# Kernel tuning notes

Measured on AMD Instinct MI355X. Metric: run time of the kernel, lower is better.

## Reference

```python
import jax, jax.numpy as jnp
import numpy as np

C = 1.0      # base manifold curvature (Lorentz c)
C_E = 1.0    # expert manifold curvature (all experts init to c=1.0)
K = 1        # n_activated_experts (top-k)
SCALE = 2.0  # LResNet scale for shared-expert combine
EPS = 1e-8


def _lorentz_swiglu(x, W1, W3, W2, c_mid, c_out, prescale):
    """LorentzExpert / LorentzFeedForward: SwiGLU on space coords with Lorentz time lift.
    x: [T, D] (full Lorentz vector). W1,W3: [I-1, D]; W2: [D-1, I]. Returns [T, D]."""
    if prescale:
        x = x * np.float32(np.sqrt(C_E / C))  # x * sqrt(c_expert / c)
    s1 = jax.nn.silu(x @ W1.T)                 # [T, I-1] w1(x, return_space=True)
    s3 = x @ W3.T                              # [T, I-1] w3(x, return_space=True)
    sp = s1 * s3                               # gated space part
    t = jnp.sqrt(jnp.clip((sp * sp).sum(-1, keepdims=True) + c_mid, EPS))
    h = jnp.concatenate([t, sp], axis=-1)      # [T, I] point on expert manifold
    o = h @ W2.T                               # [T, D-1] w2 space output
    ot = jnp.sqrt(jnp.clip((o * o).sum(-1, keepdims=True) + c_out, EPS))
    return jnp.concatenate([ot, o], axis=-1)   # [T, D] on base manifold


def setup_inputs() -> dict:
    key = jax.random.key(0)
    ks = jax.random.split(key, 9)
    T, D, E, I = 2048, 1024, 8, 1024
    x = jax.random.normal(ks[0], (T, D), jnp.float32)
    gate_w = jax.random.normal(ks[1], (E, D - 1), jnp.float32) / np.sqrt(D - 1)
    gate_b = jax.random.normal(ks[2], (E,), jnp.float32) * 0.01
    W1 = jax.random.normal(ks[3], (E, I - 1, D), jnp.float32) / np.sqrt(D)
    W3 = jax.random.normal(ks[4], (E, I - 1, D), jnp.float32) / np.sqrt(D)
    W2 = jax.random.normal(ks[5], (E, D - 1, I), jnp.float32) / np.sqrt(I)
    Ws1 = jax.random.normal(ks[6], (I - 1, D), jnp.float32) / np.sqrt(D)
    Ws3 = jax.random.normal(ks[7], (I - 1, D), jnp.float32) / np.sqrt(D)
    Ws2 = jax.random.normal(ks[8], (D - 1, I), jnp.float32) / np.sqrt(I)
    return {"x": x, "gate_w": gate_w, "gate_b": gate_b, "W1": W1, "W3": W3,
            "W2": W2, "Ws1": Ws1, "Ws3": Ws3, "Ws2": Ws2}


def reference(x, gate_w, gate_b, W1, W3, W2, Ws1, Ws3, Ws2):
    T, D = x.shape
    E = gate_w.shape[0]
    # ---- Gate (softmax scoring, n_groups == 1, route_scale == 1.0) ----
    logits = x[:, 1:] @ gate_w.T                                    # [T, E]
    scores = jax.nn.softmax(logits.astype(jnp.float32), axis=-1)
    biased = scores + gate_b                                        # bias only affects routing
    _, idx = jax.lax.top_k(biased, K)                               # [T, K]
    weights = jnp.take_along_axis(scores, idx, axis=-1).astype(x.dtype)  # [T, K]
    # dense per-token expert gate weights [T, E]
    oh = jax.nn.one_hot(idx, E, dtype=x.dtype)                      # [T, K, E]
    gw = (oh * weights[..., None]).sum(axis=1)                      # [T, E]
    # ---- y init: project(zeros) -> [sqrt(c), 0, ..., 0] ----
    y0 = jnp.concatenate([jnp.full((T, 1), np.sqrt(C), x.dtype),
                          jnp.zeros((T, D - 1), x.dtype)], axis=-1)
    # ---- routed experts (dense reference: every expert on every token, masked combine) ----
    e_out = jax.vmap(lambda w1, w3, w2: _lorentz_swiglu(x, w1, w3, w2, C_E, C, True))(W1, W3, W2)  # [E, T, D]
    y = y0 + jnp.einsum('te,etd->td', gw, e_out)
    # ---- shared expert (LorentzFeedForward, stays on base manifold) ----
    z = _lorentz_swiglu(x, Ws1, Ws3, Ws2, C, C, False)
    # ---- LResNet weighted sum: normalize (z + scale*y) back to manifold ----
    comb = z + SCALE * y
    li = (comb[:, 1:] ** 2).sum(-1, keepdims=True) - comb[:, :1] ** 2  # Lorentz inner <comb,comb>
    out = np.float32(np.sqrt(C)) * comb / jnp.sqrt(jnp.clip(jnp.abs(li), EPS))
    return out
```

## Files before the change

### kernel.cpp

```cpp
#include <hip/hip_runtime.h>

typedef __bf16 bf16;
typedef __attribute__((ext_vector_type(8))) __bf16 bf16x8;
typedef __attribute__((ext_vector_type(4))) float floatx4;

#define TOK 2048
#define DD  1024
#define NE  8
#define SMAX 24

#define MFMA16(A,B,C) __builtin_amdgcn_mfma_f32_16x16x32_bf16(A,B,C,0,0,0)

__device__ __forceinline__ void load_lds16(const bf16* g, bf16* l) {
  __builtin_amdgcn_global_load_lds(
      (const __attribute__((address_space(1))) void*)g,
      (__attribute__((address_space(3))) void*)l, 16, 0, 0);
}

#define WBAR(N) asm volatile("s_waitcnt vmcnt(" #N ")\n\ts_barrier" ::: "memory")
#define BARO    asm volatile("s_barrier" ::: "memory")

__device__ __forceinline__ uint4 pack_bf8(float4 a, float4 b) {
  union { bf16 h[8]; uint4 u; } p;
  p.h[0] = (bf16)a.x; p.h[1] = (bf16)a.y; p.h[2] = (bf16)a.z; p.h[3] = (bf16)a.w;
  p.h[4] = (bf16)b.x; p.h[5] = (bf16)b.y; p.h[6] = (bf16)b.z; p.h[7] = (bf16)b.w;
  return p.u;
}

#define NCVT (8*2046 + 2046 + 8*1023 + 1023)
__global__ __launch_bounds__(128) void convert_kernel(
    const float* __restrict__ W1, const float* __restrict__ W3,
    const float* __restrict__ W2, const float* __restrict__ Ws1,
    const float* __restrict__ Ws3, const float* __restrict__ Ws2,
    bf16* __restrict__ w13, bf16* __restrict__ ws13,
    bf16* __restrict__ w2b, bf16* __restrict__ ws2b)
{
  const int r = blockIdx.x, tid = threadIdx.x;
  const float* src; bf16* dst;
  if (r < 8 * 2046) {
    const int e = r / 2046, q = r % 2046;
    src = ((q & 1) ? W3 : W1) + ((size_t)e * 1023 + (q >> 1)) * 1024;
    dst = w13 + (size_t)r * 1024;
  } else if (r < 8 * 2046 + 2046) {
    const int q = r - 8 * 2046;
    src = ((q & 1) ? Ws3 : Ws1) + (size_t)(q >> 1) * 1024;
    dst = ws13 + (size_t)q * 1024;
  } else if (r < 8 * 2046 + 2046 + 8 * 1023) {
    const int q = r - (8 * 2046 + 2046);
    src = W2 + (size_t)q * 1024;
    dst = w2b + (size_t)q * 1024;
  } else {
    const int q = r - (8 * 2046 + 2046 + 8 * 1023);
    src = Ws2 + (size_t)q * 1024;
    dst = ws2b + (size_t)q * 1024;
  }
  const float4 f0 = ((const float4*)src)[tid * 2];
  const float4 f1 = ((const float4*)src)[tid * 2 + 1];
  ((uint4*)dst)[tid] = pack_bf8(f0, f1);
}

__global__ __launch_bounds__(256) void gate_cvt_kernel(
    const float* __restrict__ x, const float* __restrict__ gate_w,
    const float* __restrict__ gate_b, bf16* __restrict__ x_bf,
    int* __restrict__ eidx, float* __restrict__ ewgt, float* __restrict__ ss)
{
  const int t = blockIdx.x, tid = threadIdx.x;
  if (tid < 4) ss[tid * TOK + t] = 0.f;
  const float4 v = ((const float4*)(x + (size_t)t * DD))[tid];
  union { bf16 h[4]; uint2 u; } pk;
  pk.h[0] = (bf16)v.x; pk.h[1] = (bf16)v.y; pk.h[2] = (bf16)v.z; pk.h[3] = (bf16)v.w;
  ((uint2*)(x_bf + (size_t)t * DD))[tid] = pk.u;

  float acc[NE];
#pragma unroll
  for (int e = 0; e < NE; ++e) acc[e] = 0.f;
  const float vv[4] = {v.x, v.y, v.z, v.w};
#pragma unroll
  for (int i = 0; i < 4; ++i) {
    const int d = tid * 4 + i;
    if (d >= 1) {
#pragma unroll
      for (int e = 0; e < NE; ++e) acc[e] += vv[i] * gate_w[e * (DD - 1) + d - 1];
    }
  }
#pragma unroll
  for (int off = 32; off > 0; off >>= 1) {
#pragma unroll
    for (int e = 0; e < NE; ++e) acc[e] += __shfl_down(acc[e], off);
  }
  __shared__ float red[4][NE];
  const int wid = tid >> 6, lane = tid & 63;
  if (lane == 0) {
#pragma unroll
    for (int e = 0; e < NE; ++e) red[wid][e] = acc[e];
  }
  __syncthreads();
  if (tid == 0) {
    float lg[NE];
#pragma unroll
    for (int e = 0; e < NE; ++e) lg[e] = red[0][e] + red[1][e] + red[2][e] + red[3][e];
    float m = lg[0];
    for (int e = 1; e < NE; ++e) m = fmaxf(m, lg[e]);
    float ex[NE], s = 0.f;
    for (int e = 0; e < NE; ++e) { ex[e] = expf(lg[e] - m); s += ex[e]; }
    const float inv = 1.f / s;
    int best = 0; float bb = ex[0] * inv + gate_b[0];
    for (int e = 1; e < NE; ++e) {
      const float b = ex[e] * inv + gate_b[e];
      if (b > bb) { bb = b; best = e; }
    }
    eidx[t] = best;
    ewgt[t] = ex[best] * inv;
  }
}

__global__ __launch_bounds__(256) void route_kernel(
    const int* __restrict__ eidx, int* __restrict__ perm,
    int* __restrict__ pos_of, int4* __restrict__ wl, int* __restrict__ n1)
{
  __shared__ int cnt[NE], off[NE], bas[NE + 1];
  const int tid = threadIdx.x;
  if (tid < NE) cnt[tid] = 0;
  __syncthreads();
  for (int t = tid; t < TOK; t += 256) atomicAdd(&cnt[eidx[t]], 1);
  __syncthreads();
  if (tid == 0) {
    int run = 0;
    for (int e = 0; e < NE; ++e) { bas[e] = run; off[e] = run; run += cnt[e]; }
    bas[NE] = run;
    int n = 0;
    for (int e = 0; e < NE; ++e)
      for (int r0 = 0; r0 < cnt[e]; r0 += 256) {
        int rows = cnt[e] - r0; if (rows > 256) rows = 256;
        wl[n++] = make_int4(bas[e] + r0, rows, e, 0);
      }
    for (int r0 = 0; r0 < TOK; r0 += 256) wl[n++] = make_int4(r0, 256, NE, 0);
    *n1 = n;
  }
  __syncthreads();
  for (int t = tid; t < TOK; t += 256) {
    const int e = eidx[t];
    const int p = atomicAdd(&off[e], 1);
    perm[p] = t;
    pos_of[t] = p;
  }
}

__global__ __launch_bounds__(1024) void mlp1_kernel(
    const bf16* __restrict__ x_bf, const bf16* __restrict__ w13,
    const bf16* __restrict__ ws13,
    const int* __restrict__ perm, const int4* __restrict__ wl,
    const int* __restrict__ wl_n,
    bf16* __restrict__ h_r, bf16* __restrict__ h_s,
    float* __restrict__ ss_r, float* __restrict__ ss_z)
{
  const int bid = blockIdx.x;
  const int slot = bid % SMAX, nt = bid / SMAX;
  if (slot >= *wl_n) return;
  const int4 wle = wl[slot];
  const int mbase = wle.x, rows = wle.y, eid = wle.z;
  const int tid = threadIdx.x;
  const bool routed = (eid < NE);
  const bf16* bmat = routed ? w13 + (size_t)eid * 2046 * 1024 : ws13;
  bf16* hbuf  = routed ? h_r : h_s;
  float* ssbuf = routed ? ss_r : ss_z;

  extern __shared__ __align__(16) bf16 smem[];
  bf16* const Asb[2] = {smem, smem + 16384};
  bf16* const Bsb[2] = {smem + 32768, smem + 49152};
  __shared__ int toks[256];
  if (tid < 256) {
    int r = tid < rows ? tid : rows - 1;
    toks[tid] = routed ? perm[mbase + r] : (mbase + r);
  }
  __syncthreads();

  const int wid = tid >> 6, lane = tid & 63;
  const int srow = lane >> 3;
  const int kbg  = (lane & 7) ^ (srow & 7);
  const bf16 *aG0, *aG1, *bG0, *bG1;
  int aL0o, aL1o, bL0o, bL1o;
  {
    const int r0 = wid * 16;
    aG0 = x_bf + (size_t)toks[r0 + 0 + srow] * 1024 + kbg * 8;
    aG1 = x_bf + (size_t)toks[r0 + 8 + srow] * 1024 + kbg * 8;
    aL0o = (r0 + 0) * 64; aL1o = (r0 + 8) * 64;
    int b0 = nt * 256 + r0 + 0 + srow; if (b0 > 2045) b0 = 2045;
    int b1 = nt * 256 + r0 + 8 + srow; if (b1 > 2045) b1 = 2045;
    bG0 = bmat + (size_t)b0 * 1024 + kbg * 8;
    bG1 = bmat + (size_t)b1 * 1024 + kbg * 8;
    bL0o = (r0 + 0) * 64; bL1o = (r0 + 8) * 64;
  }

  const int lrow = lane & 15, quad = lane >> 4, sw = lane & 7;
  const int wrow = (wid >> 2) * 64, wcol = (wid & 3) * 64;
  int aoff[4], boff[4], koff[2];
#pragma unroll
  for (int mi = 0; mi < 4; ++mi) aoff[mi] = (wrow + mi * 16 + lrow) * 64;
#pragma unroll
  for (int ni = 0; ni < 4; ++ni) boff[ni] = (wcol + ni * 16 + lrow) * 64;
#pragma unroll
  for (int kk = 0; kk < 2; ++kk) koff[kk] = ((kk * 4 + quad) ^ sw) * 8;

  const floatx4 fz = {0.f, 0.f, 0.f, 0.f};
  floatx4 acc[4][4];
#pragma unroll
  for (int mi = 0; mi < 4; ++mi)
#pragma unroll
    for (int ni = 0; ni < 4; ++ni) acc[mi][ni] = fz;

#define STAGE1(KE, BUF) { \
    load_lds16(aG0 + (KE), Asb[BUF] + aL0o); load_lds16(aG1 + (KE), Asb[BUF] + aL1o); \
    load_lds16(bG0 + (KE), Bsb[BUF] + bL0o); load_lds16(bG1 + (KE), Bsb[BUF] + bL1o); }

#define COMP1(BUF) { \
_Pragma("unroll") \
    for (int kk = 0; kk < 2; ++kk) { \
      bf16x8 av[4], bv[4]; \
_Pragma("unroll") \
      for (int mi = 0; mi < 4; ++mi) av[mi] = *(const bf16x8*)(Asb[BUF] + aoff[mi] + koff[kk]); \
_Pragma("unroll") \
      for (int ni = 0; ni < 4; ++ni) bv[ni] = *(const bf16x8*)(Bsb[BUF] + boff[ni] + koff[kk]); \
_Pragma("unroll") \
      for (int mi = 0; mi < 4; ++mi) \
_Pragma("unroll") \
        for (int ni = 0; ni < 4; ++ni) \
          acc[mi][ni] = MFMA16(av[mi], bv[ni], acc[mi][ni]); \
    } }

  STAGE1(0, 0)
  STAGE1(64, 1)
#pragma unroll 1
  for (int t = 0; t < 7; ++t) {
    const int ke = t * 128;
    WBAR(4); COMP1(0) BARO; STAGE1(ke + 128, 0)
    WBAR(4); COMP1(1) BARO; STAGE1(ke + 192, 1)
  }
  WBAR(4); COMP1(0)
  WBAR(0); COMP1(1)
#undef STAGE1
#undef COMP1

#pragma unroll
  for (int mi = 0; mi < 4; ++mi) {
#pragma unroll
    for (int r = 0; r < 4; ++r) {
      const int row = wrow + mi * 16 + quad * 4 + r;
      const bool rowok = row < rows;
      float ssum = 0.f;
#pragma unroll
      for (int ni = 0; ni < 4; ++ni) {
        const float c = acc[mi][ni][r];
        const float partner = __shfl_xor(c, 1);
        const float s1 = (lane & 1) ? partner : c;
        const float s3 = (lane & 1) ? c : partner;
        const float sp = (s1 / (1.f + __expf(-s1))) * s3;
        const int P = (nt * 256 + wcol + ni * 16 + lrow) >> 1;
        const bool ok = rowok && ((lane & 1) == 0) && (P < 1023);
        if (ok) hbuf[(size_t)(mbase + row) * 1024 + 1 + P] = (bf16)sp;
        ssum += ok ? sp * sp : 0.f;
      }
      ssum += __shfl_xor(ssum, 1);
      ssum += __shfl_xor(ssum, 2);
      ssum += __shfl_xor(ssum, 4);
      ssum += __shfl_xor(ssum, 8);
      if (lrow == 0 && rowok) atomicAdd(ssbuf + mbase + row, ssum);
    }
  }
}

__global__ __launch_bounds__(256) void finalize_t_kernel(
    const float* __restrict__ ss_r, const float* __restrict__ ss_z,
    bf16* __restrict__ h_r, bf16* __restrict__ h_s)
{
  const int i = blockIdx.x * 256 + threadIdx.x;
  if (i < TOK) {
    h_r[(size_t)i * 1024] = (bf16)sqrtf(ss_r[i] + 1.0f);
    h_s[(size_t)i * 1024] = (bf16)sqrtf(ss_z[i] + 1.0f);
  }
}

__global__ __launch_bounds__(1024) void mlp2_kernel(
    const bf16* __restrict__ h_r, const bf16* __restrict__ h_s,
    const bf16* __restrict__ w2b, const bf16* __restrict__ ws2b,
    const int4* __restrict__ wl, const int* __restrict__ wl_n,
    float* __restrict__ o_r, float* __restrict__ o_s,
    float* __restrict__ ss_or, float* __restrict__ ss_oz)
{
  const int bid = blockIdx.x;
  const int slot = bid % SMAX, nt = bid / SMAX;
  if (slot >= *wl_n) return;
  const int4 wle = wl[slot];
  const int mbase = wle.x, rows = wle.y, eid = wle.z;
  const int tid = threadIdx.x;
  const bool routed = (eid < NE);
  const bf16* abuf = routed ? h_r : h_s;
  const bf16* bmat = routed ? w2b + (size_t)eid * 1023 * 1024 : ws2b;
  float* obuf  = routed ? o_r : o_s;
  float* ssbuf = routed ? ss_or : ss_oz;
  const int n0 = nt * 256;

  extern __shared__ __align__(16) bf16 smem[];
  bf16* const Asb[2] = {smem, smem + 16384};
  bf16* const Bsb[2] = {smem + 32768, smem + 49152};

  const int wid = tid >> 6, lane = tid & 63;
  const int srow = lane >> 3;
  const int kbg  = (lane & 7) ^ (srow & 7);
  const bf16 *aG0, *aG1, *bG0, *bG1;
  int aL0o, aL1o, bL0o, bL1o;
  {
    const int r0 = wid * 16;
    int ra0 = r0 + 0 + srow; if (ra0 >= rows) ra0 = rows - 1;
    int ra1 = r0 + 8 + srow; if (ra1 >= rows) ra1 = rows - 1;
    aG0 = abuf + (size_t)(mbase + ra0) * 1024 + kbg * 8;
    aG1 = abuf + (size_t)(mbase + ra1) * 1024 + kbg * 8;
    aL0o = (r0 + 0) * 64; aL1o = (r0 + 8) * 64;
    int b0 = n0 + r0 + 0 + srow; if (b0 > 1022) b0 = 1022;
    int b1 = n0 + r0 + 8 + srow; if (b1 > 1022) b1 = 1022;
    bG0 = bmat + (size_t)b0 * 1024 + kbg * 8;
    bG1 = bmat + (size_t)b1 * 1024 + kbg * 8;
    bL0o = (r0 + 0) * 64; bL1o = (r0 + 8) * 64;
  }

  const int lrow = lane & 15, quad = lane >> 4, sw = lane & 7;
  const int wrow = (wid >> 2) * 64, wcol = (wid & 3) * 64;
  int aoff[4], boff[4], koff[2];
#pragma unroll
  for (int mi = 0; mi < 4; ++mi) aoff[mi] = (wrow + mi * 16 + lrow) * 64;
#pragma unroll
  for (int ni = 0; ni < 4; ++ni) boff[ni] = (wcol + ni * 16 + lrow) * 64;
#pragma unroll
  for (int kk = 0; kk < 2; ++kk) koff[kk] = ((kk * 4 + quad) ^ sw) * 8;

  const floatx4 fz = {0.f, 0.f, 0.f, 0.f};
  floatx4 acc[4][4];
#pragma unroll
  for (int mi = 0; mi < 4; ++mi)
#pragma unroll
    for (int ni = 0; ni < 4; ++ni) acc[mi][ni] = fz;

#define STAGE2(KE, BUF) { \
    load_lds16(aG0 + (KE), Asb[BUF] + aL0o); load_lds16(aG1 + (KE), Asb[BUF] + aL1o); \
    load_lds16(bG0 + (KE), Bsb[BUF] + bL0o); load_lds16(bG1 + (KE), Bsb[BUF] + bL1o); }

#define COMP2(BUF) { \
_Pragma("unroll") \
    for (int kk = 0; kk < 2; ++kk) { \
      bf16x8 av[4], bv[4]; \
_Pragma("unroll") \
      for (int mi = 0; mi < 4; ++mi) av[mi] = *(const bf16x8*)(Asb[BUF] + aoff[mi] + koff[kk]); \
_Pragma("unroll") \
      for (int ni = 0; ni < 4; ++ni) bv[ni] = *(const bf16x8*)(Bsb[BUF] + boff[ni] + koff[kk]); \
_Pragma("unroll") \
      for (int mi = 0; mi < 4; ++mi) \
_Pragma("unroll") \
        for (int ni = 0; ni < 4; ++ni) \
          acc[mi][ni] = MFMA16(av[mi], bv[ni], acc[mi][ni]); \
    } }

  STAGE2(0, 0)
  STAGE2(64, 1)
#pragma unroll 1
  for (int t = 0; t < 7; ++t) {
    const int ke = t * 128;
    WBAR(4); COMP2(0) BARO; STAGE2(ke + 128, 0)
    WBAR(4); COMP2(1) BARO; STAGE2(ke + 192, 1)
  }
  WBAR(4); COMP2(0)
  WBAR(0); COMP2(1)
#undef STAGE2
#undef COMP2

#pragma unroll
  for (int mi = 0; mi < 4; ++mi) {
#pragma unroll
    for (int r = 0; r < 4; ++r) {
      const int row = wrow + mi * 16 + quad * 4 + r;
      const bool rowok = row < rows;
      float ssum = 0.f;
#pragma unroll
      for (int ni = 0; ni < 4; ++ni) {
        const float v = acc[mi][ni][r];
        const int n = n0 + wcol + ni * 16 + lrow;
        const bool ok = rowok && (n < 1023);
        if (ok) obuf[(size_t)(mbase + row) * 1024 + n] = v;
        ssum += ok ? v * v : 0.f;
      }
      ssum += __shfl_xor(ssum, 1);
      ssum += __shfl_xor(ssum, 2);
      ssum += __shfl_xor(ssum, 4);
      ssum += __shfl_xor(ssum, 8);
      if (lrow == 0 && rowok) atomicAdd(ssbuf + mbase + row, ssum);
    }
  }
}

__global__ __launch_bounds__(256) void combine_kernel(
    const float* __restrict__ o_r, const float* __restrict__ o_s,
    const float* __restrict__ ss_or, const float* __restrict__ ss_oz,
    const int* __restrict__ pos_of, const float* __restrict__ wgt,
    float* __restrict__ out)
{
  const int t = blockIdx.x, tid = threadIdx.x;
  const int p = pos_of[t];
  const float w = wgt[t];
  const float4 oz = ((const float4*)(o_s + (size_t)t * 1024))[tid];
  const float4 oe = ((const float4*)(o_r + (size_t)p * 1024))[tid];
  const float tw = 2.f * w;
  float c0 = oz.x + tw * oe.x;
  float c1 = oz.y + tw * oe.y;
  float c2 = oz.z + tw * oe.z;
  float c3 = (tid == 255) ? 0.f : (oz.w + tw * oe.w);
  float ssum = c0 * c0 + c1 * c1 + c2 * c2 + c3 * c3;
#pragma unroll
  for (int off = 32; off > 0; off >>= 1) ssum += __shfl_down(ssum, off);
  __shared__ float rs[4];
  if ((tid & 63) == 0) rs[tid >> 6] = ssum;
  __syncthreads();
  const float space2 = rs[0] + rs[1] + rs[2] + rs[3];
  const float comb0 = sqrtf(ss_oz[t] + 1.f) + 2.f + 2.f * w * sqrtf(ss_or[p] + 1.f);
  const float li = space2 - comb0 * comb0;
  const float inv = 1.f / sqrtf(fmaxf(fabsf(li), 1e-8f));
  float* orow = out + (size_t)t * 1024;
  const int j = 1 + tid * 4;
  orow[j]     = c0 * inv;
  orow[j + 1] = c1 * inv;
  orow[j + 2] = c2 * inv;
  if (tid != 255) orow[j + 3] = c3 * inv;
  if (tid == 0) orow[0] = comb0 * inv;
}

extern "C" void kernel_launch(void* const* d_in, const int* in_sizes, int n_in,
                              void* d_out, int out_size, void* d_ws, size_t ws_size,
                              hipStream_t stream) {
  const float* x      = (const float*)d_in[0];
  const float* gate_w = (const float*)d_in[1];
  const float* gate_b = (const float*)d_in[2];
  const float* W1     = (const float*)d_in[3];
  const float* W3     = (const float*)d_in[4];
  const float* W2     = (const float*)d_in[5];
  const float* Ws1    = (const float*)d_in[6];
  const float* Ws3    = (const float*)d_in[7];
  const float* Ws2    = (const float*)d_in[8];
  float* out = (float*)d_out;

  char* ws = (char*)d_ws;
  size_t off = 0;
  auto alloc = [&](size_t bytes) {
    void* p = ws + off;
    off += (bytes + 255) & ~(size_t)255;
    return p;
  };
  bf16*  x_bf = (bf16*) alloc((size_t)TOK * 1024 * 2);
  bf16*  h_r  = (bf16*) alloc((size_t)TOK * 1024 * 2);
  bf16*  h_s  = (bf16*) alloc((size_t)TOK * 1024 * 2);
  float* o_r  = (float*)alloc((size_t)TOK * 1024 * 4);
  float* o_s  = (float*)alloc((size_t)TOK * 1024 * 4);
  float* ss   = (float*)alloc((size_t)4 * TOK * 4);
  int*   eidx = (int*)  alloc((size_t)TOK * 4);
  float* ewgt = (float*)alloc((size_t)TOK * 4);
  int*   perm = (int*)  alloc((size_t)TOK * 4);
  int*   posf = (int*)  alloc((size_t)TOK * 4);
  int4*  wl1  = (int4*) alloc((size_t)SMAX * 16);
  int*   wn   = (int*)  alloc(32);
  bf16*  w13  = (bf16*) alloc((size_t)8 * 2046 * 1024 * 2);
  bf16*  ws13 = (bf16*) alloc((size_t)2046 * 1024 * 2);
  bf16*  w2b  = (bf16*) alloc((size_t)8 * 1023 * 1024 * 2);
  bf16*  ws2b = (bf16*) alloc((size_t)1023 * 1024 * 2);

  float* ss_r  = ss;
  float* ss_z  = ss + TOK;
  float* ss_or = ss + 2 * TOK;
  float* ss_oz = ss + 3 * TOK;

  const int MLP_LDS = 2 * (256 * 64 + 256 * 64) * 2;
  (void)hipFuncSetAttribute((const void*)mlp1_kernel,
                            hipFuncAttributeMaxDynamicSharedMemorySize, MLP_LDS);
  (void)hipFuncSetAttribute((const void*)mlp2_kernel,
                            hipFuncAttributeMaxDynamicSharedMemorySize, MLP_LDS);

  convert_kernel<<<NCVT, 128, 0, stream>>>(W1, W3, W2, Ws1, Ws3, Ws2,
                                           w13, ws13, w2b, ws2b);
  gate_cvt_kernel<<<TOK, 256, 0, stream>>>(x, gate_w, gate_b, x_bf, eidx, ewgt, ss);
  route_kernel<<<1, 256, 0, stream>>>(eidx, perm, posf, wl1, wn);
  mlp1_kernel<<<8 * SMAX, 1024, MLP_LDS, stream>>>(x_bf, w13, ws13, perm, wl1, wn,
                                                   h_r, h_s, ss_r, ss_z);
  finalize_t_kernel<<<8, 256, 0, stream>>>(ss_r, ss_z, h_r, h_s);
  mlp2_kernel<<<4 * SMAX, 1024, MLP_LDS, stream>>>(h_r, h_s, w2b, ws2b, wl1, wn,
                                                   o_r, o_s, ss_or, ss_oz);
  combine_kernel<<<TOK, 256, 0, stream>>>(o_r, o_s, ss_or, ss_oz, posf, ewgt, out);
}
```

Baseline: 246.1 us.

## Split-K the second MLP GEMM with atomic accumulation and merge prep kernels

The second MLP GEMM is split into two K halves, which doubles the grid and accumulates partial results into zeroed output buffers with float atomics. Because those outputs are now partial, the output squared-norm reduction moves into the combine kernel. The weight conversion, gate and zeroing work are merged into one prep kernel with 256-thread blocks that each convert one row of 1024 floats. The aim is better CU occupancy for the small mlp2 grid and fewer launches, at the cost of extra zeroing traffic and contended atomic writes.

```diff
diff --git a/kernel.cpp b/kernel.cpp
--- a/kernel.cpp
+++ b/kernel.cpp
@@ -20,52 +20,59 @@
 #define WBAR(N) asm volatile("s_waitcnt vmcnt(" #N ")\n\ts_barrier" ::: "memory")
 #define BARO    asm volatile("s_barrier" ::: "memory")
 
-__device__ __forceinline__ uint4 pack_bf8(float4 a, float4 b) {
-  union { bf16 h[8]; uint4 u; } p;
-  p.h[0] = (bf16)a.x; p.h[1] = (bf16)a.y; p.h[2] = (bf16)a.z; p.h[3] = (bf16)a.w;
-  p.h[4] = (bf16)b.x; p.h[5] = (bf16)b.y; p.h[6] = (bf16)b.z; p.h[7] = (bf16)b.w;
-  return p.u;
-}
-
 #define NCVT (8*2046 + 2046 + 8*1023 + 1023)
-__global__ __launch_bounds__(128) void convert_kernel(
+#define GATEB TOK
+#define ZEROB TOK
+__global__ __launch_bounds__(256) void prep_kernel(
+    const float* __restrict__ x, const float* __restrict__ gate_w,
+    const float* __restrict__ gate_b,
     const float* __restrict__ W1, const float* __restrict__ W3,
     const float* __restrict__ W2, const float* __restrict__ Ws1,
     const float* __restrict__ Ws3, const float* __restrict__ Ws2,
+    bf16* __restrict__ x_bf, int* __restrict__ eidx, float* __restrict__ ewgt,
+    float* __restrict__ ss,
     bf16* __restrict__ w13, bf16* __restrict__ ws13,
-    bf16* __restrict__ w2b, bf16* __restrict__ ws2b)
+    bf16* __restrict__ w2b, bf16* __restrict__ ws2b,
+    float* __restrict__ o_r, float* __restrict__ o_s)
 {
-  const int r = blockIdx.x, tid = threadIdx.x;
-  const float* src; bf16* dst;
-  if (r < 8 * 2046) {
-    const int e = r / 2046, q = r % 2046;
-    src = ((q & 1) ? W3 : W1) + ((size_t)e * 1023 + (q >> 1)) * 1024;
-    dst = w13 + (size_t)r * 1024;
-  } else if (r < 8 * 2046 + 2046) {
-    const int q = r - 8 * 2046;
-    src = ((q & 1) ? Ws3 : Ws1) + (size_t)(q >> 1) * 1024;
-    dst = ws13 + (size_t)q * 1024;
-  } else if (r < 8 * 2046 + 2046 + 8 * 1023) {
-    const int q = r - (8 * 2046 + 2046);
-    src = W2 + (size_t)q * 1024;
-    dst = w2b + (size_t)q * 1024;
-  } else {
-    const int q = r - (8 * 2046 + 2046 + 8 * 1023);
-    src = Ws2 + (size_t)q * 1024;
-    dst = ws2b + (size_t)q * 1024;
-  }
-  const float4 f0 = ((const float4*)src)[tid * 2];
-  const float4 f1 = ((const float4*)src)[tid * 2 + 1];
-  ((uint4*)dst)[tid] = pack_bf8(f0, f1);
-}
-
-__global__ __launch_bounds__(256) void gate_cvt_kernel(
-    const float* __restrict__ x, const float* __restrict__ gate_w,
-    const float* __restrict__ gate_b, bf16* __restrict__ x_bf,
-    int* __restrict__ eidx, float* __restrict__ ewgt, float* __restrict__ ss)
-{
-  const int t = blockIdx.x, tid = threadIdx.x;
-  if (tid < 4) ss[tid * TOK + t] = 0.f;
+  const int bid = blockIdx.x, tid = threadIdx.x;
+
+  if (bid >= GATEB) {
+    if (bid >= GATEB + NCVT) {
+      const int t = bid - (GATEB + NCVT);
+      const float4 z = {0.f, 0.f, 0.f, 0.f};
+      ((float4*)(o_r + (size_t)t * 1024))[tid] = z;
+      ((float4*)(o_s + (size_t)t * 1024))[tid] = z;
+      return;
+    }
+    const int r = bid - GATEB;
+    const float* src; bf16* dst;
+    if (r < 8 * 2046) {
+      const int e = r / 2046, q = r % 2046;
+      src = ((q & 1) ? W3 : W1) + ((size_t)e * 1023 + (q >> 1)) * 1024;
+      dst = w13 + (size_t)r * 1024;
+    } else if (r < 8 * 2046 + 2046) {
+      const int q = r - 8 * 2046;
+      src = ((q & 1) ? Ws3 : Ws1) + (size_t)(q >> 1) * 1024;
+      dst = ws13 + (size_t)q * 1024;
+    } else if (r < 8 * 2046 + 2046 + 8 * 1023) {
+      const int q = r - (8 * 2046 + 2046);
+      src = W2 + (size_t)q * 1024;
+      dst = w2b + (size_t)q * 1024;
+    } else {
+      const int q = r - (8 * 2046 + 2046 + 8 * 1023);
+      src = Ws2 + (size_t)q * 1024;
+      dst = ws2b + (size_t)q * 1024;
+    }
+    const float4 f = ((const float4*)src)[tid];
+    union { bf16 h[4]; uint2 u; } p;
+    p.h[0] = (bf16)f.x; p.h[1] = (bf16)f.y; p.h[2] = (bf16)f.z; p.h[3] = (bf16)f.w;
+    ((uint2*)dst)[tid] = p.u;
+    return;
+  }
+
+  const int t = bid;
+  if (tid < 2) ss[tid * TOK + t] = 0.f;
   const float4 v = ((const float4*)(x + (size_t)t * DD))[tid];
   union { bf16 h[4]; uint2 u; } pk;
   pk.h[0] = (bf16)v.x; pk.h[1] = (bf16)v.y; pk.h[2] = (bf16)v.z; pk.h[3] = (bf16)v.w;
@@ -284,11 +291,12 @@
     const bf16* __restrict__ h_r, const bf16* __restrict__ h_s,
     const bf16* __restrict__ w2b, const bf16* __restrict__ ws2b,
     const int4* __restrict__ wl, const int* __restrict__ wl_n,
-    float* __restrict__ o_r, float* __restrict__ o_s,
-    float* __restrict__ ss_or, float* __restrict__ ss_oz)
+    float* __restrict__ o_r, float* __restrict__ o_s)
 {
   const int bid = blockIdx.x;
-  const int slot = bid % SMAX, nt = bid / SMAX;
+  const int slot = bid % SMAX;
+  const int rest = bid / SMAX;
+  const int nt = rest & 3, kh = rest >> 2;
   if (slot >= *wl_n) return;
   const int4 wle = wl[slot];
   const int mbase = wle.x, rows = wle.y, eid = wle.z;
@@ -296,9 +304,9 @@
   const bool routed = (eid < NE);
   const bf16* abuf = routed ? h_r : h_s;
   const bf16* bmat = routed ? w2b + (size_t)eid * 1023 * 1024 : ws2b;
-  float* obuf  = routed ? o_r : o_s;
-  float* ssbuf = routed ? ss_or : ss_oz;
+  float* obuf = routed ? o_r : o_s;
   const int n0 = nt * 256;
+  const int kbase = kh * 512;
 
   extern __shared__ __align__(16) bf16 smem[];
   bf16* const Asb[2] = {smem, smem + 16384};
@@ -313,13 +321,13 @@
     const int r0 = wid * 16;
     int ra0 = r0 + 0 + srow; if (ra0 >= rows) ra0 = rows - 1;
     int ra1 = r0 + 8 + srow; if (ra1 >= rows) ra1 = rows - 1;
-    aG0 = abuf + (size_t)(mbase + ra0) * 1024 + kbg * 8;
-    aG1 = abuf + (size_t)(mbase + ra1) * 1024 + kbg * 8;
+    aG0 = abuf + (size_t)(mbase + ra0) * 1024 + kbase + kbg * 8;
+    aG1 = abuf + (size_t)(mbase + ra1) * 1024 + kbase + kbg * 8;
     aL0o = (r0 + 0) * 64; aL1o = (r0 + 8) * 64;
     int b0 = n0 + r0 + 0 + srow; if (b0 > 1022) b0 = 1022;
     int b1 = n0 + r0 + 8 + srow; if (b1 > 1022) b1 = 1022;
-    bG0 = bmat + (size_t)b0 * 1024 + kbg * 8;
-    bG1 = bmat + (size_t)b1 * 1024 + kbg * 8;
+    bG0 = bmat + (size_t)b0 * 1024 + kbase + kbg * 8;
+    bG1 = bmat + (size_t)b1 * 1024 + kbase + kbg * 8;
     bL0o = (r0 + 0) * 64; bL1o = (r0 + 8) * 64;
   }
 
@@ -362,7 +370,7 @@
   STAGE2(0, 0)
   STAGE2(64, 1)
 #pragma unroll 1
-  for (int t = 0; t < 7; ++t) {
+  for (int t = 0; t < 3; ++t) {
     const int ke = t * 128;
     WBAR(4); COMP2(0) BARO; STAGE2(ke + 128, 0)
     WBAR(4); COMP2(1) BARO; STAGE2(ke + 192, 1)
@@ -377,28 +385,20 @@
 #pragma unroll
     for (int r = 0; r < 4; ++r) {
       const int row = wrow + mi * 16 + quad * 4 + r;
-      const bool rowok = row < rows;
-      float ssum = 0.f;
-#pragma unroll
-      for (int ni = 0; ni < 4; ++ni) {
-        const float v = acc[mi][ni][r];
-        const int n = n0 + wcol + ni * 16 + lrow;
-        const bool ok = rowok && (n < 1023);
-        if (ok) obuf[(size_t)(mbase + row) * 1024 + n] = v;
-        ssum += ok ? v * v : 0.f;
+      if (row < rows) {
+        float* orow = obuf + (size_t)(mbase + row) * 1024;
+#pragma unroll
+        for (int ni = 0; ni < 4; ++ni) {
+          const int n = n0 + wcol + ni * 16 + lrow;
+          if (n < 1023) atomicAdd(orow + n, acc[mi][ni][r]);
+        }
       }
-      ssum += __shfl_xor(ssum, 1);
-      ssum += __shfl_xor(ssum, 2);
-      ssum += __shfl_xor(ssum, 4);
-      ssum += __shfl_xor(ssum, 8);
-      if (lrow == 0 && rowok) atomicAdd(ssbuf + mbase + row, ssum);
     }
   }
 }
 
 __global__ __launch_bounds__(256) void combine_kernel(
     const float* __restrict__ o_r, const float* __restrict__ o_s,
-    const float* __restrict__ ss_or, const float* __restrict__ ss_oz,
     const int* __restrict__ pos_of, const float* __restrict__ wgt,
     float* __restrict__ out)
 {
@@ -412,14 +412,24 @@
   float c1 = oz.y + tw * oe.y;
   float c2 = oz.z + tw * oe.z;
   float c3 = (tid == 255) ? 0.f : (oz.w + tw * oe.w);
-  float ssum = c0 * c0 + c1 * c1 + c2 * c2 + c3 * c3;
-#pragma unroll
-  for (int off = 32; off > 0; off >>= 1) ssum += __shfl_down(ssum, off);
-  __shared__ float rs[4];
-  if ((tid & 63) == 0) rs[tid >> 6] = ssum;
+  float sc = c0 * c0 + c1 * c1 + c2 * c2 + c3 * c3;
+  float sz = oz.x * oz.x + oz.y * oz.y + oz.z * oz.z + ((tid == 255) ? 0.f : oz.w * oz.w);
+  float sr = oe.x * oe.x + oe.y * oe.y + oe.z * oe.z + ((tid == 255) ? 0.f : oe.w * oe.w);
+#pragma unroll
+  for (int off = 32; off > 0; off >>= 1) {
+    sc += __shfl_down(sc, off);
+    sz += __shfl_down(sz, off);
+    sr += __shfl_down(sr, off);
+  }
+  __shared__ float rs[3][4];
+  if ((tid & 63) == 0) {
+    rs[0][tid >> 6] = sc; rs[1][tid >> 6] = sz; rs[2][tid >> 6] = sr;
+  }
   __syncthreads();
-  const float space2 = rs[0] + rs[1] + rs[2] + rs[3];
-  const float comb0 = sqrtf(ss_oz[t] + 1.f) + 2.f + 2.f * w * sqrtf(ss_or[p] + 1.f);
+  const float space2 = rs[0][0] + rs[0][1] + rs[0][2] + rs[0][3];
+  const float ss_oz  = rs[1][0] + rs[1][1] + rs[1][2] + rs[1][3];
+  const float ss_or  = rs[2][0] + rs[2][1] + rs[2][2] + rs[2][3];
+  const float comb0 = sqrtf(ss_oz + 1.f) + 2.f + 2.f * w * sqrtf(ss_or + 1.f);
   const float li = space2 - comb0 * comb0;
   const float inv = 1.f / sqrtf(fmaxf(fabsf(li), 1e-8f));
   float* orow = out + (size_t)t * 1024;
@@ -457,7 +467,7 @@
   bf16*  h_s  = (bf16*) alloc((size_t)TOK * 1024 * 2);
   float* o_r  = (float*)alloc((size_t)TOK * 1024 * 4);
   float* o_s  = (float*)alloc((size_t)TOK * 1024 * 4);
-  float* ss   = (float*)alloc((size_t)4 * TOK * 4);
+  float* ss   = (float*)alloc((size_t)2 * TOK * 4);
   int*   eidx = (int*)  alloc((size_t)TOK * 4);
   float* ewgt = (float*)alloc((size_t)TOK * 4);
   int*   perm = (int*)  alloc((size_t)TOK * 4);
@@ -471,8 +481,6 @@
 
   float* ss_r  = ss;
   float* ss_z  = ss + TOK;
-  float* ss_or = ss + 2 * TOK;
-  float* ss_oz = ss + 3 * TOK;
 
   const int MLP_LDS = 2 * (256 * 64 + 256 * 64) * 2;
   (void)hipFuncSetAttribute((const void*)mlp1_kernel,
@@ -480,14 +488,14 @@
   (void)hipFuncSetAttribute((const void*)mlp2_kernel,
                             hipFuncAttributeMaxDynamicSharedMemorySize, MLP_LDS);
 
-  convert_kernel<<<NCVT, 128, 0, stream>>>(W1, W3, W2, Ws1, Ws3, Ws2,
-                                           w13, ws13, w2b, ws2b);
-  gate_cvt_kernel<<<TOK, 256, 0, stream>>>(x, gate_w, gate_b, x_bf, eidx, ewgt, ss);
+  prep_kernel<<<GATEB + NCVT + ZEROB, 256, 0, stream>>>(
+      x, gate_w, gate_b, W1, W3, W2, Ws1, Ws3, Ws2,
+      x_bf, eidx, ewgt, ss, w13, ws13, w2b, ws2b, o_r, o_s);
   route_kernel<<<1, 256, 0, stream>>>(eidx, perm, posf, wl1, wn);
   mlp1_kernel<<<8 * SMAX, 1024, MLP_LDS, stream>>>(x_bf, w13, ws13, perm, wl1, wn,
                                                    h_r, h_s, ss_r, ss_z);
   finalize_t_kernel<<<8, 256, 0, stream>>>(ss_r, ss_z, h_r, h_s);
-  mlp2_kernel<<<4 * SMAX, 1024, MLP_LDS, stream>>>(h_r, h_s, w2b, ws2b, wl1, wn,
-                                                   o_r, o_s, ss_or, ss_oz);
-  combine_kernel<<<TOK, 256, 0, stream>>>(o_r, o_s, ss_or, ss_oz, posf, ewgt, out);
-}
+  mlp2_kernel<<<8 * SMAX, 1024, MLP_LDS, stream>>>(h_r, h_s, w2b, ws2b, wl1, wn,
+                                                   o_r, o_s);
+  combine_kernel<<<TOK, 256, 0, stream>>>(o_r, o_s, posf, ewgt, out);
+}
```

Result: no change. 248.1 us (+0.8%).
